# Kernel optimization log

Hardware: AMD Instinct MI355X
Metric: run time of the kernel (lower is better)

The kernel has to match this reference:

```python
import jax, jax.numpy as jnp
import numpy as np

N_NODES = 50000
N_EDGES = 800000
IN_CH = 128
EDGE_DIM = 16
HID = 64
HEADS = 2
OUT = 64


def _transformer_conv(x, src, dst, edge_attr, Wq, bq, Wk, bk, Wv, bv, We, Ws, bs, H, C):
    # PyG TransformerConv, eval mode, concat=True, root_weight=True, beta=False.
    N = x.shape[0]
    q = (x @ Wq + bq).reshape(N, H, C)
    k = (x @ Wk + bk).reshape(N, H, C)
    v = (x @ Wv + bv).reshape(N, H, C)
    e = (edge_attr @ We).reshape(-1, H, C)          # [E,H,C], lin_edge has no bias
    kj = k[src] + e                                  # gather + edge-aware key
    vj = v[src] + e                                  # gather + edge-aware value
    alpha = jnp.einsum('ehc,ehc->eh', q[dst], kj) / jnp.sqrt(jnp.asarray(C, x.dtype))
    # segment softmax over incoming edges of each target node
    m = jax.ops.segment_max(alpha, dst, num_segments=N)
    m = jnp.where(jnp.isfinite(m), m, jnp.zeros_like(m))
    ex = jnp.exp(alpha - m[dst])
    den = jax.ops.segment_sum(ex, dst, num_segments=N)
    a = ex / (den[dst] + 1e-16)                      # [E,H]
    agg = jax.ops.segment_sum(a[:, :, None] * vj, dst, num_segments=N)  # [N,H,C]
    return agg.reshape(N, H * C) + (x @ Ws + bs)     # concat heads + root skip


def setup_inputs() -> dict:
    key = jax.random.key(0)
    ks = jax.random.split(key, 24)
    s = 0.05
    d1 = HEADS * HID   # 128
    d2 = 1 * OUT       # 64
    inp = {
        'x': jax.random.normal(ks[0], (N_NODES, IN_CH), jnp.float32),
        'edge_index': jax.random.randint(ks[1], (2, N_EDGES), 0, N_NODES, jnp.int32),
        'edge_attr': jax.random.normal(ks[2], (N_EDGES, EDGE_DIM), jnp.float32),
        # layer 1 params
        'Wq1': jax.random.normal(ks[3], (IN_CH, d1), jnp.float32) * s,
        'bq1': jnp.zeros((d1,), jnp.float32),
        'Wk1': jax.random.normal(ks[4], (IN_CH, d1), jnp.float32) * s,
        'bk1': jnp.zeros((d1,), jnp.float32),
        'Wv1': jax.random.normal(ks[5], (IN_CH, d1), jnp.float32) * s,
        'bv1': jnp.zeros((d1,), jnp.float32),
        'We1': jax.random.normal(ks[6], (EDGE_DIM, d1), jnp.float32) * s,
        'Ws1': jax.random.normal(ks[7], (IN_CH, d1), jnp.float32) * s,
        'bs1': jnp.zeros((d1,), jnp.float32),
        # layer 2 params (heads=1)
        'Wq2': jax.random.normal(ks[8], (d1, d2), jnp.float32) * s,
        'bq2': jnp.zeros((d2,), jnp.float32),
        'Wk2': jax.random.normal(ks[9], (d1, d2), jnp.float32) * s,
        'bk2': jnp.zeros((d2,), jnp.float32),
        'Wv2': jax.random.normal(ks[10], (d1, d2), jnp.float32) * s,
        'bv2': jnp.zeros((d2,), jnp.float32),
        'We2': jax.random.normal(ks[11], (EDGE_DIM, d2), jnp.float32) * s,
        'Ws2': jax.random.normal(ks[12], (d1, d2), jnp.float32) * s,
        'bs2': jnp.zeros((d2,), jnp.float32),
    }
    return inp


def reference(x, edge_index, edge_attr,
              Wq1, bq1, Wk1, bk1, Wv1, bv1, We1, Ws1, bs1,
              Wq2, bq2, Wk2, bk2, Wv2, bv2, We2, Ws2, bs2):
    src, dst = edge_index[0], edge_index[1]
    h = _transformer_conv(x, src, dst, edge_attr,
                          Wq1, bq1, Wk1, bk1, Wv1, bv1, We1, Ws1, bs1, HEADS, HID)
    h = jax.nn.relu(h)
    out = _transformer_conv(h, src, dst, edge_attr,
                            Wq2, bq2, Wk2, bk2, Wv2, bv2, We2, Ws2, bs2, 1, OUT)
    return out
```

## Files before the change

### kernel.cpp

```cpp
#include <hip/hip_runtime.h>
#include <hip/hip_bf16.h>

#define NN 50000
#define NE 800000
#define NSCB 196

#define PB_HIST  3125
#define PB_PW1   (PB_HIST + 32)
#define PB_PW2   (PB_PW1 + 16)
#define PB_PA1   (PB_PW2 + 2)
#define PB_PA2   (PB_PA1 + 1)

typedef __attribute__((ext_vector_type(8))) short bf16x8;
typedef __attribute__((ext_vector_type(4))) float f32x4;

__device__ __forceinline__ float2 bfp(uint32_t u) {
    union { uint32_t i; float f; } lo, hi;
    lo.i = u << 16;
    hi.i = u & 0xffff0000u;
    return make_float2(lo.f, hi.f);
}
__device__ __forceinline__ float bf1(uint16_t u) {
    union { uint32_t i; float f; } x; x.i = ((uint32_t)u) << 16; return x.f;
}
__device__ __forceinline__ float4 bfp4(uint32_t a, uint32_t b) {
    const float2 lo = bfp(a), hi = bfp(b);
    return make_float4(lo.x, lo.y, hi.x, hi.y);
}

__device__ __forceinline__ void hist_dev(int e, const int* __restrict__ dst,
                                         int* __restrict__ cnt)
{
    if (e < NE) atomicAdd(&cnt[dst[e]], 1);
}

template<int M>
__device__ __forceinline__ void pack_w_dev(
    int t, const float* __restrict__ Wq, const float* __restrict__ Wk,
    const float* __restrict__ Wv, const float* __restrict__ Wsk,
    const float* __restrict__ bq, const float* __restrict__ bk,
    const float* __restrict__ bv, const float* __restrict__ bsk,
    __hip_bfloat16* __restrict__ Wp, float* __restrict__ bcat)
{
    constexpr int NFQ = M / 16;
    constexpr int NF_TOT = 4 * NFQ;
    if (t >= 4 * NF_TOT * 64) return;
    const int l  = t & 63;
    const int fg = (t >> 6) % NF_TOT;
    const int s  = t / (64 * NF_TOT);
    const int sec = fg / NFQ;
    const int fl  = fg % NFQ;
    const float* W = sec == 0 ? Wq : sec == 1 ? Wk : sec == 2 ? Wv : Wsk;
    const int col = fl * 16 + (l & 15);
    const int k0  = s * 32 + (l >> 4) * 8;
    __hip_bfloat16 tmp[8];
    #pragma unroll
    for (int j = 0; j < 8; ++j) tmp[j] = __float2bfloat16(W[(size_t)(k0 + j) * M + col]);
    *reinterpret_cast<uint4*>(Wp + ((size_t)(fg * 4 + s) * 64 + l) * 8) =
        *reinterpret_cast<const uint4*>(tmp);
    if (s == 0 && (l >> 4) == 0) {
        const float* B = sec == 0 ? bq : sec == 1 ? bk : sec == 2 ? bv : bsk;
        bcat[fg * 16 + (l & 15)] = B[col];
    }
}

template<int MW, int MO>
__device__ __forceinline__ void pack_wq_dev(
    int t, const float* __restrict__ Wq, const float* __restrict__ We,
    const float* __restrict__ bq,
    __hip_bfloat16* __restrict__ Ap, float* __restrict__ B0)
{
    constexpr int NF = MO / 16;
    if (t >= 4 * NF * 64) return;
    const int l  = t & 63;
    const int fg = (t >> 6) % NF;
    const int s  = t / (64 * NF);
    const int col = fg * 16 + (l & 15);
    const int h = col >> 4;
    const int r = col & 15;
    const int k0 = s * 32 + (l >> 4) * 8;
    __hip_bfloat16 tmp[8];
    #pragma unroll
    for (int jj = 0; jj < 8; ++jj) {
        float acc = 0.f;
        for (int c = 0; c < 64; ++c)
            acc += Wq[(size_t)(k0 + jj) * MW + h * 64 + c] * We[r * MW + h * 64 + c];
        tmp[jj] = __float2bfloat16(acc * 0.125f);
    }
    *reinterpret_cast<uint4*>(Ap + ((size_t)(fg * 4 + s) * 64 + l) * 8) =
        *reinterpret_cast<const uint4*>(tmp);
    if (s == 0 && (l >> 4) == 0) {
        float acc = 0.f;
        for (int c = 0; c < 64; ++c) acc += bq[h * 64 + c] * We[r * MW + h * 64 + c];
        B0[col] = acc * 0.125f;
    }
}

__global__ __launch_bounds__(256)
void prep(const int* __restrict__ dstp, int* __restrict__ cnt,
          const float* Wq1, const float* Wk1, const float* Wv1, const float* Ws1,
          const float* bq1, const float* bk1, const float* bv1, const float* bs1,
          const float* We1,
          const float* Wq2, const float* Wk2, const float* Wv2, const float* Ws2,
          const float* bq2, const float* bk2, const float* bv2, const float* bs2,
          const float* We2,
          __hip_bfloat16* Wp1, float* bcat1,
          __hip_bfloat16* Wp2, float* bcat2)
{
    const int b = blockIdx.x;
    const int tid = threadIdx.x;
    if (b < PB_HIST) {
        hist_dev(b * 256 + tid, dstp, cnt);
    } else if (b < PB_PW1) {
        pack_w_dev<128>((b - PB_HIST) * 256 + tid, Wq1, Wk1, Wv1, Ws1,
                        bq1, bk1, bv1, bs1, Wp1, bcat1);
    } else if (b < PB_PW2) {
        pack_w_dev<64>((b - PB_PW1) * 256 + tid, Wq2, Wk2, Wv2, Ws2,
                       bq2, bk2, bv2, bs2, Wp2, bcat2);
    } else if (b < PB_PA1) {
        pack_wq_dev<128, 32>((b - PB_PW2) * 256 + tid, Wq1, We1, bq1,
                             Wp1 + (size_t)32 * 2048, bcat1 + 512);
    } else {
        pack_wq_dev<64, 16>((b - PB_PA1) * 256 + tid, Wq2, We2, bq2,
                            Wp2 + (size_t)16 * 2048, bcat2 + 256);
    }
}

template<int M, int MO, bool F32IN>
__global__ __launch_bounds__(256)
void gemm_fused(const void* __restrict__ xin,
                const __hip_bfloat16* __restrict__ Wp,
                const float* __restrict__ bcat,
                __hip_bfloat16* __restrict__ q, __hip_bfloat16* __restrict__ kv,
                __hip_bfloat16* __restrict__ skip, float* __restrict__ wqo)
{
    constexpr int NF_TOT = (4 * M + MO) / 16;
    constexpr int NFW = (NF_TOT + 3) / 4;
    const int wid  = threadIdx.x >> 6;
    const int l    = threadIdx.x & 63;
    const int row0 = blockIdx.x * 16;
    const int rowg = row0 + (l & 15);
    const int kb   = l >> 4;

    f32x4 acc[NFW];
    #pragma unroll
    for (int f = 0; f < NFW; ++f) acc[f] = f32x4{0.f, 0.f, 0.f, 0.f};

    const bf16x8* wp8 = reinterpret_cast<const bf16x8*>(Wp);
    #pragma unroll
    for (int s = 0; s < 4; ++s) {
        bf16x8 a;
        if constexpr (F32IN) {
            const float* xf = (const float*)xin;
            const float4 a0 = *reinterpret_cast<const float4*>(
                xf + (size_t)rowg * 128 + s * 32 + kb * 8);
            const float4 a1 = *reinterpret_cast<const float4*>(
                xf + (size_t)rowg * 128 + s * 32 + kb * 8 + 4);
            union { __hip_bfloat16 h[8]; bf16x8 v; } u;
            u.h[0] = __float2bfloat16(a0.x); u.h[1] = __float2bfloat16(a0.y);
            u.h[2] = __float2bfloat16(a0.z); u.h[3] = __float2bfloat16(a0.w);
            u.h[4] = __float2bfloat16(a1.x); u.h[5] = __float2bfloat16(a1.y);
            u.h[6] = __float2bfloat16(a1.z); u.h[7] = __float2bfloat16(a1.w);
            a = u.v;
        } else {
            const __hip_bfloat16* xb = (const __hip_bfloat16*)xin;
            a = *reinterpret_cast<const bf16x8*>(xb + (size_t)rowg * 128 + s * 32 + kb * 8);
        }
        #pragma unroll
        for (int f = 0; f < NFW; ++f) {
            const int fg = wid + 4 * f;
            if (fg < NF_TOT)
                acc[f] = __builtin_amdgcn_mfma_f32_16x16x32_bf16(
                    a, wp8[(size_t)(fg * 4 + s) * 64 + l], acc[f], 0, 0, 0);
        }
    }

    const int cl = l & 15;
    #pragma unroll
    for (int f = 0; f < NFW; ++f) {
        const int fg = wid + 4 * f;
        if (fg >= NF_TOT) continue;
        const int cg = fg * 16 + cl;
        const float bb = bcat[cg];
        #pragma unroll
        for (int j = 0; j < 4; ++j) {
            const int row = row0 + kb * 4 + j;
            const float val = acc[f][j] + bb;
            if (cg < M) {
                q[(size_t)row * M + cg] = __float2bfloat16(val * 0.125f);
            } else if (cg < 2 * M) {
                const int c = cg - M;
                kv[(size_t)row * 2 * M + (c >> 2) * 8 + (c & 3)] = __float2bfloat16(val);
            } else if (cg < 3 * M) {
                const int c = cg - 2 * M;
                kv[(size_t)row * 2 * M + (c >> 2) * 8 + 4 + (c & 3)] = __float2bfloat16(val);
            } else if (cg < 4 * M) {
                skip[(size_t)row * M + (cg - 3 * M)] = __float2bfloat16(val);
            } else {
                wqo[(size_t)row * MO + (cg - 4 * M)] = val;
            }
        }
    }
}

__global__ __launch_bounds__(256)
void scan_blk(const int* __restrict__ cnt, int* __restrict__ inc, int* __restrict__ bsum)
{
    __shared__ int s[256];
    const int idx = blockIdx.x * 256 + threadIdx.x;
    const int v = (idx < NN) ? cnt[idx] : 0;
    s[threadIdx.x] = v;
    __syncthreads();
    #pragma unroll
    for (int d = 1; d < 256; d <<= 1) {
        const int t = (threadIdx.x >= d) ? s[threadIdx.x - d] : 0;
        __syncthreads();
        s[threadIdx.x] += t;
        __syncthreads();
    }
    if (idx < NN) inc[idx] = s[threadIdx.x];
    if (threadIdx.x == 255) bsum[blockIdx.x] = s[255];
}

__global__ __launch_bounds__(256)
void scan_top(const int* __restrict__ bsum, int* __restrict__ boff)
{
    __shared__ int s[256];
    const int v = (threadIdx.x < NSCB) ? bsum[threadIdx.x] : 0;
    s[threadIdx.x] = v;
    __syncthreads();
    #pragma unroll
    for (int d = 1; d < 256; d <<= 1) {
        const int t = (threadIdx.x >= d) ? s[threadIdx.x - d] : 0;
        __syncthreads();
        s[threadIdx.x] += t;
        __syncthreads();
    }
    boff[threadIdx.x] = s[threadIdx.x] - v;
}

__global__ __launch_bounds__(256)
void scan_fin(const int* __restrict__ cnt, const int* __restrict__ inc,
              const int* __restrict__ boff, int* __restrict__ off, int* __restrict__ cursor)
{
    const int idx = blockIdx.x * 256 + threadIdx.x;
    if (idx < NN) {
        const int o = inc[idx] - cnt[idx] + boff[blockIdx.x];
        off[idx] = o;
        cursor[idx] = o;
    }
    if (idx == 0) off[NN] = NE;
}

__global__ __launch_bounds__(256)
void scatter_edges(const int* __restrict__ dst, const int* __restrict__ src,
                   const float* __restrict__ ea, int* __restrict__ cursor,
                   int* __restrict__ srcs, __hip_bfloat16* __restrict__ eap)
{
    const int e = blockIdx.x * 256 + threadIdx.x;
    if (e >= NE) return;
    const int p = atomicAdd(&cursor[dst[e]], 1);
    srcs[p] = src[e];
    const float4* ea4 = reinterpret_cast<const float4*>(ea) + (size_t)e * 4;
    const float4 a0 = ea4[0], a1 = ea4[1], a2 = ea4[2], a3 = ea4[3];
    const float af[16] = {a0.x,a0.y,a0.z,a0.w, a1.x,a1.y,a1.z,a1.w,
                          a2.x,a2.y,a2.z,a2.w, a3.x,a3.y,a3.z,a3.w};
    __hip_bfloat16 tmp[16];
    #pragma unroll
    for (int r = 0; r < 16; ++r) tmp[r] = __float2bfloat16(af[r]);
    uint4* dp = reinterpret_cast<uint4*>(eap + (size_t)p * 16);
    dp[0] = *reinterpret_cast<const uint4*>(&tmp[0]);
    dp[1] = *reinterpret_cast<const uint4*>(&tmp[8]);
}

__global__ __launch_bounds__(256)
void agg_l1(const int* __restrict__ off, const int* __restrict__ srcs,
            const __hip_bfloat16* __restrict__ eap,
            const float* __restrict__ We,
            const float* __restrict__ wq,
            const __hip_bfloat16* __restrict__ qb,
            const __hip_bfloat16* __restrict__ kv,
            const __hip_bfloat16* __restrict__ skb,
            __hip_bfloat16* __restrict__ hb)
{
    __shared__ float wes[16 * 128];
    for (int i = threadIdx.x; i < 16 * 128; i += 256) wes[i] = We[i];
    __syncthreads();

    const int node = blockIdx.x * 4 + (threadIdx.x >> 6);
    const int lane = threadIdx.x & 63;
    const int hf   = lane >> 5;
    const int hl   = lane & 31;
    const int g    = lane & 15;
    const int ch   = hl * 4;

    const size_t nb = (size_t)node * 128;
    const uint16_t* qu = reinterpret_cast<const uint16_t*>(qb);
    const uint2 qw = *reinterpret_cast<const uint2*>(qu + nb + ch);
    const float4 qv = bfp4(qw.x, qw.y);
    const float wqv = wq[(size_t)node * 32 + (hl >> 4) * 16 + g];
    const uint16_t* kvu = reinterpret_cast<const uint16_t*>(kv);
    const uint16_t* eau = reinterpret_cast<const uint16_t*>(eap);

    float acc0 = 0.f, acc1 = 0.f, acc2 = 0.f, acc3 = 0.f, den = 0.f, eacc = 0.f;
    const int beg = off[node], end = off[node + 1];

    for (int i = beg; i < end; i += 8) {
        const int ii0 = i + hf,     ii1 = i + 2 + hf;
        const int ii2 = i + 4 + hf, ii3 = i + 6 + hf;
        const bool v0 = ii0 < end, v1 = ii1 < end, v2 = ii2 < end, v3 = ii3 < end;
        const int i0 = v0 ? ii0 : beg, i1 = v1 ? ii1 : beg;
        const int i2 = v2 ? ii2 : beg, i3 = v3 ? ii3 : beg;
        const int s0 = srcs[i0], s1 = srcs[i1], s2 = srcs[i2], s3 = srcs[i3];
        const uint4 x0 = *reinterpret_cast<const uint4*>(kvu + (size_t)s0 * 256 + hl * 8);
        const uint4 x1 = *reinterpret_cast<const uint4*>(kvu + (size_t)s1 * 256 + hl * 8);
        const uint4 x2 = *reinterpret_cast<const uint4*>(kvu + (size_t)s2 * 256 + hl * 8);
        const uint4 x3 = *reinterpret_cast<const uint4*>(kvu + (size_t)s3 * 256 + hl * 8);
        const float ea0 = bf1(eau[(size_t)i0 * 16 + g]);
        const float ea1 = bf1(eau[(size_t)i1 * 16 + g]);
        const float ea2 = bf1(eau[(size_t)i2 * 16 + g]);
        const float ea3 = bf1(eau[(size_t)i3 * 16 + g]);
        const float4 k0 = bfp4(x0.x, x0.y), k1 = bfp4(x1.x, x1.y);
        const float4 k2 = bfp4(x2.x, x2.y), k3 = bfp4(x3.x, x3.y);
        float p0 = fmaf(qv.x, k0.x, fmaf(qv.y, k0.y,
                   fmaf(qv.z, k0.z, fmaf(qv.w, k0.w, ea0 * wqv))));
        float p1 = fmaf(qv.x, k1.x, fmaf(qv.y, k1.y,
                   fmaf(qv.z, k1.z, fmaf(qv.w, k1.w, ea1 * wqv))));
        float p2 = fmaf(qv.x, k2.x, fmaf(qv.y, k2.y,
                   fmaf(qv.z, k2.z, fmaf(qv.w, k2.w, ea2 * wqv))));
        float p3 = fmaf(qv.x, k3.x, fmaf(qv.y, k3.y,
                   fmaf(qv.z, k3.z, fmaf(qv.w, k3.w, ea3 * wqv))));
        #pragma unroll
        for (int m = 1; m < 16; m <<= 1) {
            p0 += __shfl_xor(p0, m, 64);
            p1 += __shfl_xor(p1, m, 64);
            p2 += __shfl_xor(p2, m, 64);
            p3 += __shfl_xor(p3, m, 64);
        }
        const float ex0 = v0 ? __expf(p0) : 0.f;
        const float ex1 = v1 ? __expf(p1) : 0.f;
        const float ex2 = v2 ? __expf(p2) : 0.f;
        const float ex3 = v3 ? __expf(p3) : 0.f;
        const float4 w0 = bfp4(x0.z, x0.w), w1 = bfp4(x1.z, x1.w);
        const float4 w2 = bfp4(x2.z, x2.w), w3 = bfp4(x3.z, x3.w);
        acc0 = fmaf(ex0, w0.x, fmaf(ex1, w1.x, fmaf(ex2, w2.x, fmaf(ex3, w3.x, acc0))));
        acc1 = fmaf(ex0, w0.y, fmaf(ex1, w1.y, fmaf(ex2, w2.y, fmaf(ex3, w3.y, acc1))));
        acc2 = fmaf(ex0, w0.z, fmaf(ex1, w1.z, fmaf(ex2, w2.z, fmaf(ex3, w3.z, acc2))));
        acc3 = fmaf(ex0, w0.w, fmaf(ex1, w1.w, fmaf(ex2, w2.w, fmaf(ex3, w3.w, acc3))));
        den += (ex0 + ex1) + (ex2 + ex3);
        eacc = fmaf(ex0, ea0, fmaf(ex1, ea1, fmaf(ex2, ea2, fmaf(ex3, ea3, eacc))));
    }

    acc0 += __shfl_xor(acc0, 32, 64);
    acc1 += __shfl_xor(acc1, 32, 64);
    acc2 += __shfl_xor(acc2, 32, 64);
    acc3 += __shfl_xor(acc3, 32, 64);
    den  += __shfl_xor(den, 32, 64);
    eacc += __shfl_xor(eacc, 32, 64);

    const int gb = lane & 16;
    #pragma unroll
    for (int r = 0; r < 16; ++r) {
        const float er = __shfl(eacc, gb + r, 64);
        const float4 w = *reinterpret_cast<const float4*>(&wes[r * 128 + ch]);
        acc0 = fmaf(er, w.x, acc0);
        acc1 = fmaf(er, w.y, acc1);
        acc2 = fmaf(er, w.z, acc2);
        acc3 = fmaf(er, w.w, acc3);
    }

    if (hf == 0) {
        const float inv = 1.f / (den + 1e-16f);
        const uint16_t* sku = reinterpret_cast<const uint16_t*>(skb);
        const uint2 skw = *reinterpret_cast<const uint2*>(sku + nb + ch);
        const float4 sk = bfp4(skw.x, skw.y);
        __hip_bfloat16 hp[4] = {
            __float2bfloat16(fmaxf(fmaf(acc0, inv, sk.x), 0.f)),
            __float2bfloat16(fmaxf(fmaf(acc1, inv, sk.y), 0.f)),
            __float2bfloat16(fmaxf(fmaf(acc2, inv, sk.z), 0.f)),
            __float2bfloat16(fmaxf(fmaf(acc3, inv, sk.w), 0.f))};
        *reinterpret_cast<uint2*>(hb + nb + ch) = *reinterpret_cast<const uint2*>(hp);
    }
}

__global__ __launch_bounds__(256)
void agg_l2(const int* __restrict__ off, const int* __restrict__ srcs,
            const __hip_bfloat16* __restrict__ eap,
            const float* __restrict__ We,
            const float* __restrict__ wq,
            const __hip_bfloat16* __restrict__ qb,
            const __hip_bfloat16* __restrict__ kv,
            const __hip_bfloat16* __restrict__ skb,
            float* __restrict__ out)
{
    __shared__ float wes[16 * 64];
    for (int i = threadIdx.x; i < 16 * 64; i += 256) wes[i] = We[i];
    __syncthreads();

    const int node = blockIdx.x * 4 + (threadIdx.x >> 6);
    const int lane = threadIdx.x & 63;
    const int grp  = lane >> 4;
    const int g    = lane & 15;
    const int ch   = g * 4;

    const size_t nb = (size_t)node * 64;
    const uint16_t* qu = reinterpret_cast<const uint16_t*>(qb);
    const uint2 qw = *reinterpret_cast<const uint2*>(qu + nb + ch);
    const float4 qv = bfp4(qw.x, qw.y);
    const float wqv = wq[(size_t)node * 16 + g];
    const uint16_t* kvu = reinterpret_cast<const uint16_t*>(kv);
    const uint16_t* eau = reinterpret_cast<const uint16_t*>(eap);

    float acc0 = 0.f, acc1 = 0.f, acc2 = 0.f, acc3 = 0.f, den = 0.f, eacc = 0.f;
    const int beg = off[node], end = off[node + 1];

    for (int i = beg; i < end; i += 16) {
        const int ii0 = i + grp,      ii1 = i + 4 + grp;
        const int ii2 = i + 8 + grp,  ii3 = i + 12 + grp;
        const bool v0 = ii0 < end, v1 = ii1 < end, v2 = ii2 < end, v3 = ii3 < end;
        const int i0 = v0 ? ii0 : beg, i1 = v1 ? ii1 : beg;
        const int i2 = v2 ? ii2 : beg, i3 = v3 ? ii3 : beg;
        const int s0 = srcs[i0], s1 = srcs[i1], s2 = srcs[i2], s3 = srcs[i3];
        const uint4 x0 = *reinterpret_cast<const uint4*>(kvu + (size_t)s0 * 128 + g * 8);
        const uint4 x1 = *reinterpret_cast<const uint4*>(kvu + (size_t)s1 * 128 + g * 8);
        const uint4 x2 = *reinterpret_cast<const uint4*>(kvu + (size_t)s2 * 128 + g * 8);
        const uint4 x3 = *reinterpret_cast<const uint4*>(kvu + (size_t)s3 * 128 + g * 8);
        const float ea0 = bf1(eau[(size_t)i0 * 16 + g]);
        const float ea1 = bf1(eau[(size_t)i1 * 16 + g]);
        const float ea2 = bf1(eau[(size_t)i2 * 16 + g]);
        const float ea3 = bf1(eau[(size_t)i3 * 16 + g]);
        const float4 k0 = bfp4(x0.x, x0.y), k1 = bfp4(x1.x, x1.y);
        const float4 k2 = bfp4(x2.x, x2.y), k3 = bfp4(x3.x, x3.y);
        float p0 = fmaf(qv.x, k0.x, fmaf(qv.y, k0.y,
                   fmaf(qv.z, k0.z, fmaf(qv.w, k0.w, ea0 * wqv))));
        float p1 = fmaf(qv.x, k1.x, fmaf(qv.y, k1.y,
                   fmaf(qv.z, k1.z, fmaf(qv.w, k1.w, ea1 * wqv))));
        float p2 = fmaf(qv.x, k2.x, fmaf(qv.y, k2.y,
                   fmaf(qv.z, k2.z, fmaf(qv.w, k2.w, ea2 * wqv))));
        float p3 = fmaf(qv.x, k3.x, fmaf(qv.y, k3.y,
                   fmaf(qv.z, k3.z, fmaf(qv.w, k3.w, ea3 * wqv))));
        #pragma unroll
        for (int m = 1; m < 16; m <<= 1) {
            p0 += __shfl_xor(p0, m, 64);
            p1 += __shfl_xor(p1, m, 64);
            p2 += __shfl_xor(p2, m, 64);
            p3 += __shfl_xor(p3, m, 64);
        }
        const float ex0 = v0 ? __expf(p0) : 0.f;
        const float ex1 = v1 ? __expf(p1) : 0.f;
        const float ex2 = v2 ? __expf(p2) : 0.f;
        const float ex3 = v3 ? __expf(p3) : 0.f;
        const float4 w0 = bfp4(x0.z, x0.w), w1 = bfp4(x1.z, x1.w);
        const float4 w2 = bfp4(x2.z, x2.w), w3 = bfp4(x3.z, x3.w);
        acc0 = fmaf(ex0, w0.x, fmaf(ex1, w1.x, fmaf(ex2, w2.x, fmaf(ex3, w3.x, acc0))));
        acc1 = fmaf(ex0, w0.y, fmaf(ex1, w1.y, fmaf(ex2, w2.y, fmaf(ex3, w3.y, acc1))));
        acc2 = fmaf(ex0, w0.z, fmaf(ex1, w1.z, fmaf(ex2, w2.z, fmaf(ex3, w3.z, acc2))));
        acc3 = fmaf(ex0, w0.w, fmaf(ex1, w1.w, fmaf(ex2, w2.w, fmaf(ex3, w3.w, acc3))));
        den += (ex0 + ex1) + (ex2 + ex3);
        eacc = fmaf(ex0, ea0, fmaf(ex1, ea1, fmaf(ex2, ea2, fmaf(ex3, ea3, eacc))));
    }

    acc0 += __shfl_xor(acc0, 16, 64);  acc0 += __shfl_xor(acc0, 32, 64);
    acc1 += __shfl_xor(acc1, 16, 64);  acc1 += __shfl_xor(acc1, 32, 64);
    acc2 += __shfl_xor(acc2, 16, 64);  acc2 += __shfl_xor(acc2, 32, 64);
    acc3 += __shfl_xor(acc3, 16, 64);  acc3 += __shfl_xor(acc3, 32, 64);
    den  += __shfl_xor(den, 16, 64);   den  += __shfl_xor(den, 32, 64);
    eacc += __shfl_xor(eacc, 16, 64);  eacc += __shfl_xor(eacc, 32, 64);

    #pragma unroll
    for (int r = 0; r < 16; ++r) {
        const float er = __shfl(eacc, r, 64);
        const float4 w = *reinterpret_cast<const float4*>(&wes[r * 64 + ch]);
        acc0 = fmaf(er, w.x, acc0);
        acc1 = fmaf(er, w.y, acc1);
        acc2 = fmaf(er, w.z, acc2);
        acc3 = fmaf(er, w.w, acc3);
    }

    if (lane < 16) {
        const float inv = 1.f / (den + 1e-16f);
        const uint16_t* sku = reinterpret_cast<const uint16_t*>(skb);
        const uint2 skw = *reinterpret_cast<const uint2*>(sku + nb + ch);
        const float4 sk = bfp4(skw.x, skw.y);
        *reinterpret_cast<float4*>(out + nb + ch) =
            make_float4(fmaf(acc0, inv, sk.x), fmaf(acc1, inv, sk.y),
                        fmaf(acc2, inv, sk.z), fmaf(acc3, inv, sk.w));
    }
}

extern "C" void kernel_launch(void* const* d_in, const int* in_sizes, int n_in,
                              void* d_out, int out_size, void* d_ws, size_t ws_size,
                              hipStream_t stream) {
    const float* x     = (const float*)d_in[0];
    const int*   ei    = (const int*)  d_in[1];
    const float* eattr = (const float*)d_in[2];
    const float* Wq1 = (const float*)d_in[3],  *bq1 = (const float*)d_in[4];
    const float* Wk1 = (const float*)d_in[5],  *bk1 = (const float*)d_in[6];
    const float* Wv1 = (const float*)d_in[7],  *bv1 = (const float*)d_in[8];
    const float* We1 = (const float*)d_in[9];
    const float* Ws1 = (const float*)d_in[10], *bs1 = (const float*)d_in[11];
    const float* Wq2 = (const float*)d_in[12], *bq2 = (const float*)d_in[13];
    const float* Wk2 = (const float*)d_in[14], *bk2 = (const float*)d_in[15];
    const float* Wv2 = (const float*)d_in[16], *bv2 = (const float*)d_in[17];
    const float* We2 = (const float*)d_in[18];
    const float* Ws2 = (const float*)d_in[19], *bs2 = (const float*)d_in[20];

    const int* srcp = ei;
    const int* dstp = ei + NE;

    char* base = (char*)d_ws;
    size_t o = 0;
    auto alloc = [&](size_t bytes) -> void* {
        void* p = base + o;
        o = (o + bytes + 511) & ~(size_t)511;
        return p;
    };
    float* wq1   = (float*)alloc((size_t)NN * 32 * 4);
    float* wq2   = (float*)alloc((size_t)NN * 16 * 4);
    float* bcat1 = (float*)alloc(544 * 4);
    float* bcat2 = (float*)alloc(272 * 4);
    int* srcs    = (int*)alloc((size_t)NE * 4);
    int* cnt     = (int*)alloc((size_t)NN * 4);
    int* inc     = (int*)alloc((size_t)NN * 4);
    int* off     = (int*)alloc((size_t)(NN + 1) * 4);
    int* cursor  = (int*)alloc((size_t)NN * 4);
    int* bsum    = (int*)alloc(256 * 4);
    int* boff    = (int*)alloc(256 * 4);
    __hip_bfloat16* q1b  = (__hip_bfloat16*)alloc((size_t)NN * 128 * 2);
    __hip_bfloat16* sk1b = (__hip_bfloat16*)alloc((size_t)NN * 128 * 2);
    __hip_bfloat16* hb   = (__hip_bfloat16*)alloc((size_t)NN * 128 * 2);
    __hip_bfloat16* kv1  = (__hip_bfloat16*)alloc((size_t)NN * 256 * 2);
    __hip_bfloat16* eap  = (__hip_bfloat16*)alloc((size_t)NE * 16 * 2);
    __hip_bfloat16* Wp1  = (__hip_bfloat16*)alloc((size_t)34 * 2048 * 2);
    __hip_bfloat16* Wp2  = (__hip_bfloat16*)alloc((size_t)17 * 2048 * 2);
    __hip_bfloat16* q2b  = q1b;
    __hip_bfloat16* sk2b = sk1b;
    __hip_bfloat16* kv2  = kv1;

    hipMemsetAsync(cnt, 0, (size_t)NN * sizeof(int), stream);
    prep<<<PB_PA2, 256, 0, stream>>>(dstp, cnt,
        Wq1, Wk1, Wv1, Ws1, bq1, bk1, bv1, bs1, We1,
        Wq2, Wk2, Wv2, Ws2, bq2, bk2, bv2, bs2, We2,
        Wp1, bcat1, Wp2, bcat2);

    scan_blk<<<NSCB, 256, 0, stream>>>(cnt, inc, bsum);
    scan_top<<<1, 256, 0, stream>>>(bsum, boff);
    scan_fin<<<NSCB, 256, 0, stream>>>(cnt, inc, boff, off, cursor);
    scatter_edges<<<NE / 256, 256, 0, stream>>>(dstp, srcp, eattr, cursor, srcs, eap);

    gemm_fused<128, 32, true><<<NN / 16, 256, 0, stream>>>(
        x, Wp1, bcat1, q1b, kv1, sk1b, wq1);
    agg_l1<<<NN / 4, 256, 0, stream>>>(off, srcs, eap, We1, wq1, q1b, kv1, sk1b, hb);

    gemm_fused<64, 16, false><<<NN / 16, 256, 0, stream>>>(
        hb, Wp2, bcat2, q2b, kv2, sk2b, wq2);
    agg_l2<<<NN / 4, 256, 0, stream>>>(off, srcs, eap, We2, wq2, q2b, kv2, sk2b, (float*)d_out);
}
```

Baseline: 300.8 us.

## Merge edge scatter with layer-1 GEMM, fold scan_top into scan_fin, narrow agg_l2 unroll

```diff
diff --git a/kernel.cpp b/kernel.cpp
--- a/kernel.cpp
+++ b/kernel.cpp
@@ -10,6 +10,9 @@
 #define PB_PW2   (PB_PW1 + 16)
 #define PB_PA1   (PB_PW2 + 2)
 #define PB_PA2   (PB_PA1 + 1)
+
+#define MB_SCT   3125
+#define MB_GEMM  (MB_SCT + 3125)
 
 typedef __attribute__((ext_vector_type(8))) short bf16x8;
 typedef __attribute__((ext_vector_type(4))) float f32x4;
@@ -127,18 +130,18 @@
 }
 
 template<int M, int MO, bool F32IN>
-__global__ __launch_bounds__(256)
-void gemm_fused(const void* __restrict__ xin,
-                const __hip_bfloat16* __restrict__ Wp,
-                const float* __restrict__ bcat,
-                __hip_bfloat16* __restrict__ q, __hip_bfloat16* __restrict__ kv,
-                __hip_bfloat16* __restrict__ skip, float* __restrict__ wqo)
+__device__ __forceinline__
+void gemm_dev(int blk, int tid, const void* __restrict__ xin,
+              const __hip_bfloat16* __restrict__ Wp,
+              const float* __restrict__ bcat,
+              __hip_bfloat16* __restrict__ q, __hip_bfloat16* __restrict__ kv,
+              __hip_bfloat16* __restrict__ skip, float* __restrict__ wqo)
 {
     constexpr int NF_TOT = (4 * M + MO) / 16;
     constexpr int NFW = (NF_TOT + 3) / 4;
-    const int wid  = threadIdx.x >> 6;
-    const int l    = threadIdx.x & 63;
-    const int row0 = blockIdx.x * 16;
+    const int wid  = tid >> 6;
+    const int l    = tid & 63;
+    const int row0 = blk * 16;
     const int rowg = row0 + (l & 15);
     const int kb   = l >> 4;
 
@@ -203,61 +206,24 @@
     }
 }
 
-__global__ __launch_bounds__(256)
-void scan_blk(const int* __restrict__ cnt, int* __restrict__ inc, int* __restrict__ bsum)
-{
-    __shared__ int s[256];
-    const int idx = blockIdx.x * 256 + threadIdx.x;
-    const int v = (idx < NN) ? cnt[idx] : 0;
-    s[threadIdx.x] = v;
-    __syncthreads();
-    #pragma unroll
-    for (int d = 1; d < 256; d <<= 1) {
-        const int t = (threadIdx.x >= d) ? s[threadIdx.x - d] : 0;
-        __syncthreads();
-        s[threadIdx.x] += t;
-        __syncthreads();
-    }
-    if (idx < NN) inc[idx] = s[threadIdx.x];
-    if (threadIdx.x == 255) bsum[blockIdx.x] = s[255];
-}
-
-__global__ __launch_bounds__(256)
-void scan_top(const int* __restrict__ bsum, int* __restrict__ boff)
-{
-    __shared__ int s[256];
-    const int v = (threadIdx.x < NSCB) ? bsum[threadIdx.x] : 0;
-    s[threadIdx.x] = v;
-    __syncthreads();
-    #pragma unroll
-    for (int d = 1; d < 256; d <<= 1) {
-        const int t = (threadIdx.x >= d) ? s[threadIdx.x - d] : 0;
-        __syncthreads();
-        s[threadIdx.x] += t;
-        __syncthreads();
-    }
-    boff[threadIdx.x] = s[threadIdx.x] - v;
-}
-
-__global__ __launch_bounds__(256)
-void scan_fin(const int* __restrict__ cnt, const int* __restrict__ inc,
-              const int* __restrict__ boff, int* __restrict__ off, int* __restrict__ cursor)
-{
-    const int idx = blockIdx.x * 256 + threadIdx.x;
-    if (idx < NN) {
-        const int o = inc[idx] - cnt[idx] + boff[blockIdx.x];
-        off[idx] = o;
-        cursor[idx] = o;
-    }
-    if (idx == 0) off[NN] = NE;
-}
-
-__global__ __launch_bounds__(256)
-void scatter_edges(const int* __restrict__ dst, const int* __restrict__ src,
-                   const float* __restrict__ ea, int* __restrict__ cursor,
-                   int* __restrict__ srcs, __hip_bfloat16* __restrict__ eap)
-{
-    const int e = blockIdx.x * 256 + threadIdx.x;
+template<int M, int MO, bool F32IN>
+__global__ __launch_bounds__(256)
+void gemm_fused(const void* __restrict__ xin,
+                const __hip_bfloat16* __restrict__ Wp,
+                const float* __restrict__ bcat,
+                __hip_bfloat16* __restrict__ q, __hip_bfloat16* __restrict__ kv,
+                __hip_bfloat16* __restrict__ skip, float* __restrict__ wqo)
+{
+    gemm_dev<M, MO, F32IN>(blockIdx.x, threadIdx.x, xin, Wp, bcat, q, kv, skip, wqo);
+}
+
+__device__ __forceinline__
+void scatter_dev(int blk, int tid, const int* __restrict__ dst,
+                 const int* __restrict__ src, const float* __restrict__ ea,
+                 int* __restrict__ cursor, int* __restrict__ srcs,
+                 __hip_bfloat16* __restrict__ eap)
+{
+    const int e = blk * 256 + tid;
     if (e >= NE) return;
     const int p = atomicAdd(&cursor[dst[e]], 1);
     srcs[p] = src[e];
@@ -271,6 +237,65 @@
     uint4* dp = reinterpret_cast<uint4*>(eap + (size_t)p * 16);
     dp[0] = *reinterpret_cast<const uint4*>(&tmp[0]);
     dp[1] = *reinterpret_cast<const uint4*>(&tmp[8]);
+}
+
+__global__ __launch_bounds__(256)
+void mid1(const int* __restrict__ dstp, const int* __restrict__ srcp,
+          const float* __restrict__ eattr, int* __restrict__ cursor,
+          int* __restrict__ srcs, __hip_bfloat16* __restrict__ eap,
+          const float* __restrict__ x, const __hip_bfloat16* __restrict__ Wp1,
+          const float* __restrict__ bcat1, __hip_bfloat16* __restrict__ q1b,
+          __hip_bfloat16* __restrict__ kv1, __hip_bfloat16* __restrict__ sk1b,
+          float* __restrict__ wq1)
+{
+    const int b = blockIdx.x;
+    if (b < MB_SCT)
+        scatter_dev(b, threadIdx.x, dstp, srcp, eattr, cursor, srcs, eap);
+    else
+        gemm_dev<128, 32, true>(b - MB_SCT, threadIdx.x, x, Wp1, bcat1,
+                                q1b, kv1, sk1b, wq1);
+}
+
+__global__ __launch_bounds__(256)
+void scan_blk(const int* __restrict__ cnt, int* __restrict__ inc, int* __restrict__ bsum)
+{
+    __shared__ int s[256];
+    const int idx = blockIdx.x * 256 + threadIdx.x;
+    const int v = (idx < NN) ? cnt[idx] : 0;
+    s[threadIdx.x] = v;
+    __syncthreads();
+    #pragma unroll
+    for (int d = 1; d < 256; d <<= 1) {
+        const int t = (threadIdx.x >= d) ? s[threadIdx.x - d] : 0;
+        __syncthreads();
+        s[threadIdx.x] += t;
+        __syncthreads();
+    }
+    if (idx < NN) inc[idx] = s[threadIdx.x];
+    if (threadIdx.x == 255) bsum[blockIdx.x] = s[255];
+}
+
+__global__ __launch_bounds__(256)
+void scan_fin(const int* __restrict__ cnt, const int* __restrict__ inc,
+              const int* __restrict__ bsum, int* __restrict__ off,
+              int* __restrict__ cursor)
+{
+    __shared__ int sw[4];
+    const int t = threadIdx.x;
+    int v = (t < blockIdx.x) ? bsum[t] : 0;
+    #pragma unroll
+    for (int m = 1; m < 64; m <<= 1) v += __shfl_xor(v, m, 64);
+    if ((t & 63) == 0) sw[t >> 6] = v;
+    __syncthreads();
+    const int boffset = sw[0] + sw[1] + sw[2] + sw[3];
+
+    const int idx = blockIdx.x * 256 + t;
+    if (idx < NN) {
+        const int o = inc[idx] - cnt[idx] + boffset;
+        off[idx] = o;
+        cursor[idx] = o;
+    }
+    if (idx == 0) off[NN] = NE;
 }
 
 __global__ __launch_bounds__(256)
@@ -414,50 +439,34 @@
     float acc0 = 0.f, acc1 = 0.f, acc2 = 0.f, acc3 = 0.f, den = 0.f, eacc = 0.f;
     const int beg = off[node], end = off[node + 1];
 
-    for (int i = beg; i < end; i += 16) {
-        const int ii0 = i + grp,      ii1 = i + 4 + grp;
-        const int ii2 = i + 8 + grp,  ii3 = i + 12 + grp;
-        const bool v0 = ii0 < end, v1 = ii1 < end, v2 = ii2 < end, v3 = ii3 < end;
+    for (int i = beg; i < end; i += 8) {
+        const int ii0 = i + grp, ii1 = i + 4 + grp;
+        const bool v0 = ii0 < end, v1 = ii1 < end;
         const int i0 = v0 ? ii0 : beg, i1 = v1 ? ii1 : beg;
-        const int i2 = v2 ? ii2 : beg, i3 = v3 ? ii3 : beg;
-        const int s0 = srcs[i0], s1 = srcs[i1], s2 = srcs[i2], s3 = srcs[i3];
+        const int s0 = srcs[i0], s1 = srcs[i1];
         const uint4 x0 = *reinterpret_cast<const uint4*>(kvu + (size_t)s0 * 128 + g * 8);
         const uint4 x1 = *reinterpret_cast<const uint4*>(kvu + (size_t)s1 * 128 + g * 8);
-        const uint4 x2 = *reinterpret_cast<const uint4*>(kvu + (size_t)s2 * 128 + g * 8);
-        const uint4 x3 = *reinterpret_cast<const uint4*>(kvu + (size_t)s3 * 128 + g * 8);
         const float ea0 = bf1(eau[(size_t)i0 * 16 + g]);
         const float ea1 = bf1(eau[(size_t)i1 * 16 + g]);
-        const float ea2 = bf1(eau[(size_t)i2 * 16 + g]);
-        const float ea3 = bf1(eau[(size_t)i3 * 16 + g]);
         const float4 k0 = bfp4(x0.x, x0.y), k1 = bfp4(x1.x, x1.y);
-        const float4 k2 = bfp4(x2.x, x2.y), k3 = bfp4(x3.x, x3.y);
         float p0 = fmaf(qv.x, k0.x, fmaf(qv.y, k0.y,
                    fmaf(qv.z, k0.z, fmaf(qv.w, k0.w, ea0 * wqv))));
         float p1 = fmaf(qv.x, k1.x, fmaf(qv.y, k1.y,
                    fmaf(qv.z, k1.z, fmaf(qv.w, k1.w, ea1 * wqv))));
-        float p2 = fmaf(qv.x, k2.x, fmaf(qv.y, k2.y,
-                   fmaf(qv.z, k2.z, fmaf(qv.w, k2.w, ea2 * wqv))));
-        float p3 = fmaf(qv.x, k3.x, fmaf(qv.y, k3.y,
-                   fmaf(qv.z, k3.z, fmaf(qv.w, k3.w, ea3 * wqv))));
         #pragma unroll
         for (int m = 1; m < 16; m <<= 1) {
             p0 += __shfl_xor(p0, m, 64);
             p1 += __shfl_xor(p1, m, 64);
-            p2 += __shfl_xor(p2, m, 64);
-            p3 += __shfl_xor(p3, m, 64);
         }
         const float ex0 = v0 ? __expf(p0) : 0.f;
         const float ex1 = v1 ? __expf(p1) : 0.f;
-        const float ex2 = v2 ? __expf(p2) : 0.f;
-        const float ex3 = v3 ? __expf(p3) : 0.f;
         const float4 w0 = bfp4(x0.z, x0.w), w1 = bfp4(x1.z, x1.w);
-        const float4 w2 = bfp4(x2.z, x2.w), w3 = bfp4(x3.z, x3.w);
-        acc0 = fmaf(ex0, w0.x, fmaf(ex1, w1.x, fmaf(ex2, w2.x, fmaf(ex3, w3.x, acc0))));
-        acc1 = fmaf(ex0, w0.y, fmaf(ex1, w1.y, fmaf(ex2, w2.y, fmaf(ex3, w3.y, acc1))));
-        acc2 = fmaf(ex0, w0.z, fmaf(ex1, w1.z, fmaf(ex2, w2.z, fmaf(ex3, w3.z, acc2))));
-        acc3 = fmaf(ex0, w0.w, fmaf(ex1, w1.w, fmaf(ex2, w2.w, fmaf(ex3, w3.w, acc3))));
-        den += (ex0 + ex1) + (ex2 + ex3);
-        eacc = fmaf(ex0, ea0, fmaf(ex1, ea1, fmaf(ex2, ea2, fmaf(ex3, ea3, eacc))));
+        acc0 = fmaf(ex0, w0.x, fmaf(ex1, w1.x, acc0));
+        acc1 = fmaf(ex0, w0.y, fmaf(ex1, w1.y, acc1));
+        acc2 = fmaf(ex0, w0.z, fmaf(ex1, w1.z, acc2));
+        acc3 = fmaf(ex0, w0.w, fmaf(ex1, w1.w, acc3));
+        den += ex0 + ex1;
+        eacc = fmaf(ex0, ea0, fmaf(ex1, ea1, eacc));
     }
 
     acc0 += __shfl_xor(acc0, 16, 64);  acc0 += __shfl_xor(acc0, 32, 64);
@@ -525,7 +534,6 @@
     int* off     = (int*)alloc((size_t)(NN + 1) * 4);
     int* cursor  = (int*)alloc((size_t)NN * 4);
     int* bsum    = (int*)alloc(256 * 4);
-    int* boff    = (int*)alloc(256 * 4);
     __hip_bfloat16* q1b  = (__hip_bfloat16*)alloc((size_t)NN * 128 * 2);
     __hip_bfloat16* sk1b = (__hip_bfloat16*)alloc((size_t)NN * 128 * 2);
     __hip_bfloat16* hb   = (__hip_bfloat16*)alloc((size_t)NN * 128 * 2);
@@ -544,12 +552,11 @@
         Wp1, bcat1, Wp2, bcat2);
 
     scan_blk<<<NSCB, 256, 0, stream>>>(cnt, inc, bsum);
-    scan_top<<<1, 256, 0, stream>>>(bsum, boff);
-    scan_fin<<<NSCB, 256, 0, stream>>>(cnt, inc, boff, off, cursor);
-    scatter_edges<<<NE / 256, 256, 0, stream>>>(dstp, srcp, eattr, cursor, srcs, eap);
-
-    gemm_fused<128, 32, true><<<NN / 16, 256, 0, stream>>>(
-        x, Wp1, bcat1, q1b, kv1, sk1b, wq1);
+    scan_fin<<<NSCB, 256, 0, stream>>>(cnt, inc, bsum, off, cursor);
+
+    mid1<<<MB_GEMM, 256, 0, stream>>>(dstp, srcp, eattr, cursor, srcs, eap,
+                                      x, Wp1, bcat1, q1b, kv1, sk1b, wq1);
+
     agg_l1<<<NN / 4, 256, 0, stream>>>(off, srcs, eap, We1, wq1, q1b, kv1, sk1b, hb);
 
     gemm_fused<64, 16, false><<<NN / 16, 256, 0, stream>>>(
```

Result: faster. 293.3 us (-2.5%).
